# Optimization experiments

Hardware: AMD Instinct MI355X
Metric: run time of the kernel (lower is better)

Reference implementation:

```python
import jax, jax.numpy as jnp
import numpy as np
import math

K = 7
B, C, H, W = 16, 3, 256, 256
N = 50000
ANGLE = 30.0; TRANS = 0.45; SHEAR = 0.3; SCALE0, SCALE1 = 1.0, 0.5  # self.scale assumed [1.0,0.5] (upstream AutoDO)


def _bilinear(img, xs, ys):
    # img: (C,Hs,Ws); xs,ys: (Ho,Wo) pixel coords; border padding (clamp)
    Cc, Hs, Ws = img.shape
    xs = jnp.clip(xs, 0.0, Ws - 1.0)
    ys = jnp.clip(ys, 0.0, Hs - 1.0)
    x0 = jnp.floor(xs); y0 = jnp.floor(ys)
    wx = xs - x0; wy = ys - y0
    x0i = x0.astype(jnp.int32); y0i = y0.astype(jnp.int32)
    x1i = jnp.minimum(x0i + 1, Ws - 1); y1i = jnp.minimum(y0i + 1, Hs - 1)
    Ia = img[:, y0i, x0i]; Ib = img[:, y0i, x1i]
    Ic = img[:, y1i, x0i]; Id = img[:, y1i, x1i]
    return Ia * (1 - wx) * (1 - wy) + Ib * wx * (1 - wy) + Ic * (1 - wx) * wy + Id * wx * wy


def _resize(x, Ho, Wo):
    # torch F.interpolate bilinear, align_corners=False, no antialias
    Bb, Cc, Hs, Ws = x.shape
    ys = (jnp.arange(Ho, dtype=x.dtype) + 0.5) * (Hs / Ho) - 0.5
    xs = (jnp.arange(Wo, dtype=x.dtype) + 0.5) * (Ws / Wo) - 0.5
    Y, X = jnp.meshgrid(ys, xs, indexing='ij')
    return jax.vmap(lambda im: _bilinear(im, X, Y))(x)


def _warp_perspective(x, M, Ho, Wo):
    # kornia.warp_perspective: dst(p) = src(M^-1 p), bilinear, border padding, align_corners=True
    Bb, Cc, Hs, Ws = x.shape
    Minv = jnp.linalg.inv(M)  # (B,3,3)
    yy, xx = jnp.meshgrid(jnp.arange(Ho, dtype=x.dtype), jnp.arange(Wo, dtype=x.dtype), indexing='ij')
    pts = jnp.stack([xx.ravel(), yy.ravel(), jnp.ones(Ho * Wo, dtype=x.dtype)])  # (3, Ho*Wo)
    src = jnp.einsum('bij,jn->bin', Minv, pts)
    xs = (src[:, 0] / src[:, 2]).reshape(Bb, Ho, Wo)
    ys = (src[:, 1] / src[:, 2]).reshape(Bb, Ho, Wo)
    return jax.vmap(_bilinear)(x, xs, ys)


def _forward(x, paramP, paramM, gumbel_u, eps, idx):
    dt = x.dtype
    pP = jax.nn.sigmoid(paramP[:, idx])  # (K,B)
    logits = jnp.stack([jnp.log(pP).ravel(), jnp.log(1.0 - pP).ravel()], axis=1)  # (K*B,2)
    g = -jnp.log(-jnp.log(gumbel_u))
    y_soft = jax.nn.softmax(logits + g, axis=1)  # tau=1
    y_hard = jax.nn.one_hot(jnp.argmax(y_soft, axis=1), 2, dtype=y_soft.dtype)
    y = y_hard + y_soft - jax.lax.stop_gradient(y_soft)  # straight-through hard gumbel
    sP = y[:, 0].reshape(K, B)
    sM = jax.nn.sigmoid(paramM[:, idx]) * eps  # (K,B)
    ang = sP[0] * sM[0] * ANGLE
    # replicate torch's cat(W//2 * ones(B), H//2 * ones(B)).view(-1,2) layout exactly
    ctr = jnp.concatenate([jnp.full((B,), W // 2, dt), jnp.full((B,), H // 2, dt)]).reshape(-1, 2)
    sx = SCALE0 + sP[5] * sM[5] * SCALE1
    sy = SCALE0 + sP[6] * sM[6] * SCALE1
    rad = jnp.deg2rad(ang); ca = jnp.cos(rad); sa = jnp.sin(rad)
    # kornia get_rotation_matrix2d: rot=[[c,s],[-s,c]] @ diag(sx,sy); t = ctr - rot@ctr
    sr = jnp.stack([jnp.stack([ca * sx, sa * sy], -1), jnp.stack([-sa * sx, ca * sy], -1)], -2)  # (B,2,2)
    t = ctr - jnp.einsum('bij,bj->bi', sr, ctr)
    eye = jnp.broadcast_to(jnp.eye(3, dtype=dt), (B, 3, 3))
    R = eye.at[:, :2, :2].set(sr).at[:, :2, 2].set(t)
    T = eye.at[:, 0, 2].set(W * sP[1] * sM[1] * TRANS).at[:, 1, 2].set(H * sP[2] * sM[2] * TRANS)
    S = eye.at[:, 0, 1].set(sP[3] * sM[3] * SHEAR).at[:, 1, 0].set(sP[4] * sM[4] * SHEAR)
    M = S @ T @ R
    x_up = _resize(x, 4 * H, 4 * W)
    x_w = _warp_perspective(x_up, M, 4 * H, 4 * W)
    return _resize(x_w, H, W)


def setup_inputs() -> dict:
    key = jax.random.key(0)
    k1, k2, k3, k4 = jax.random.split(key, 4)
    p = 1.0 / (K - 2)
    prob_logit = math.log(p / (1.0 - p))
    m = 5.0 / 10.0
    magn_logit = math.log(m / (1.0 - m))
    return {
        'x': jax.random.uniform(k1, (B, C, H, W), jnp.float32),
        'paramP': jnp.full((K, N), prob_logit, jnp.float32),
        'paramM': jnp.full((K, N), magn_logit, jnp.float32),
        'gumbel_u': jax.random.uniform(k2, (K * B, 2), jnp.float32, minval=1e-6, maxval=1.0 - 1e-6),
        'eps': jax.random.normal(k3, (K, B), jnp.float32),
        'idx': jax.random.randint(k4, (B,), 0, N, jnp.int32),
    }


def reference(x, paramP, paramM, gumbel_u, eps, idx):
    return _forward(x, paramP, paramM, gumbel_u, eps, idx)
```

## Files before the change

### kernel.cpp

```cpp
#include <hip/hip_runtime.h>
#include <math.h>


typedef float floatx4 __attribute__((ext_vector_type(4)));

__device__ __forceinline__ floatx4 load4(const float* p) {
    floatx4 v;
    __builtin_memcpy(&v, p, sizeof(v));
    return v;
}

struct Up { int i0; float w; };

__device__ __forceinline__ Up upc(int v) {
    float u = fmaf(0.25f, (float)v, -0.375f);
    u = fminf(fmaxf(u, 0.0f), 255.0f);
    float f = floorf(u);
    Up r; r.i0 = (int)f; r.w = u - f;
    return r;
}

struct Trip { float w0, w1, w2; int base; };

__device__ __forceinline__ Trip merged3(float s) {
    float f = floorf(s);
    float fr = s - f;
    int v0 = (int)f;
    int v1 = min(v0 + 1, 1023);
    Up c0 = upc(v0), c1 = upc(v1);
    float A0 = 1.0f - fr, A1 = fr;
    float b0 = A1 * (1.0f - c1.w), b1 = A1 * c1.w;
    bool d = (c1.i0 != c0.i0);
    Trip t;
    t.w0 = A0 * (1.0f - c0.w) + (d ? 0.0f : b0);
    t.w1 = A0 * c0.w + (d ? b0 : b1);
    t.w2 = d ? b1 : 0.0f;
    t.base = c0.i0;
    return t;
}

__device__ __forceinline__ void pair_accum(
    Trip cA, Trip cB, Trip rA, Trip rB,
    const float* __restrict__ xb, float* acc)
{
    int cb = min(cA.base, cB.base);
    int rb = min(rA.base, rB.base);
    float CA[4], CB[4], RA[4], RB[4];
    bool sa_ = (cA.base != cb);
    CA[0] = sa_ ? 0.f : cA.w0;  CA[1] = sa_ ? cA.w0 : cA.w1;
    CA[2] = sa_ ? cA.w1 : cA.w2;  CA[3] = sa_ ? cA.w2 : 0.f;
    bool sb_ = (cB.base != cb);
    CB[0] = sb_ ? 0.f : cB.w0;  CB[1] = sb_ ? cB.w0 : cB.w1;
    CB[2] = sb_ ? cB.w1 : cB.w2;  CB[3] = sb_ ? cB.w2 : 0.f;
    bool ra_ = (rA.base != rb);
    RA[0] = ra_ ? 0.f : rA.w0;  RA[1] = ra_ ? rA.w0 : rA.w1;
    RA[2] = ra_ ? rA.w1 : rA.w2;  RA[3] = ra_ ? rA.w2 : 0.f;
    bool rb_ = (rB.base != rb);
    RB[0] = rb_ ? 0.f : rB.w0;  RB[1] = rb_ ? rB.w0 : rB.w1;
    RB[2] = rb_ ? rB.w1 : rB.w2;  RB[3] = rb_ ? rB.w2 : 0.f;

    float W[4][4];
#pragma unroll
    for (int r = 0; r < 4; ++r)
#pragma unroll
        for (int c = 0; c < 4; ++c)
            W[r][c] = fmaf(RB[r], CB[c], RA[r] * CA[c]);

    int base = cb;
    if (cb > 252) {
        int shift = cb - 252;
        base = 252;
        for (int s = 0; s < shift; ++s) {
#pragma unroll
            for (int r = 0; r < 4; ++r) {
                W[r][3] = W[r][2]; W[r][2] = W[r][1];
                W[r][1] = W[r][0]; W[r][0] = 0.f;
            }
        }
    }
    int e0 = rb * 256 + base;
    int e1 = min(rb + 1, 255) * 256 + base;
    int e2 = min(rb + 2, 255) * 256 + base;
    int e3 = min(rb + 3, 255) * 256 + base;
#pragma unroll
    for (int ch = 0; ch < 3; ++ch) {
        const float* pc = xb + ch * 65536;
        floatx4 L0 = load4(pc + e0);
        floatx4 L1 = load4(pc + e1);
        floatx4 L2 = load4(pc + e2);
        floatx4 L3 = load4(pc + e3);
        float s0 = fmaf(W[0][3], L0.w, fmaf(W[0][2], L0.z, fmaf(W[0][1], L0.y, W[0][0] * L0.x)));
        float s1 = fmaf(W[1][3], L1.w, fmaf(W[1][2], L1.z, fmaf(W[1][1], L1.y, W[1][0] * L1.x)));
        float s2 = fmaf(W[2][3], L2.w, fmaf(W[2][2], L2.z, fmaf(W[2][1], L2.y, W[2][0] * L2.x)));
        float s3 = fmaf(W[3][3], L3.w, fmaf(W[3][2], L3.z, fmaf(W[3][1], L3.y, W[3][0] * L3.x)));
        acc[ch] += (s0 + s1) + (s2 + s3);
    }
}

__global__ __launch_bounds__(256) void fused_warp(
    const float* __restrict__ x,
    const float* __restrict__ paramP, const float* __restrict__ paramM,
    const float* __restrict__ gumbel_u, const float* __restrict__ eps,
    const int* __restrict__ idx,
    float* __restrict__ out, int N)
{
    int b = blockIdx.z;
    int lane = threadIdx.x;
    int wid  = threadIdx.y;

    float dec = 0.f, sMv = 0.f;
    if (lane < 7) {
        int k = lane;
        int id = idx[b];
        float vP = paramP[k * N + id];
        float pP = 1.0f / (1.0f + expf(-vP));
        float l0 = logf(pP);
        float l1 = logf(1.0f - pP);
        float u0 = gumbel_u[(k * 16 + b) * 2 + 0];
        float u1 = gumbel_u[(k * 16 + b) * 2 + 1];
        float g0 = -logf(-logf(u0));
        float g1 = -logf(-logf(u1));
        dec = (l0 + g0 >= l1 + g1) ? 1.0f : 0.0f;
        float vM = paramM[k * N + id];
        float sig = 1.0f / (1.0f + expf(-vM));
        sMv = sig * eps[k * 16 + b];
    }
    float sP[7], sM[7];
#pragma unroll
    for (int k = 0; k < 7; ++k) {
        sP[k] = __shfl(dec, k, 64);
        sM[k] = __shfl(sMv, k, 64);
    }

    float ang = sP[0] * sM[0] * 30.0f;
    float rad = ang * 0.017453292519943295f;
    float ca = cosf(rad), sa = sinf(rad);
    float sx = 1.0f + sP[5] * sM[5] * 0.5f;
    float sy = 1.0f + sP[6] * sM[6] * 0.5f;
    float sr00 = ca * sx, sr01 = sa * sy;
    float sr10 = -sa * sx, sr11 = ca * sy;
    float t0 = 128.0f - (sr00 + sr01) * 128.0f;
    float t1 = 128.0f - (sr10 + sr11) * 128.0f;
    float tx2 = 256.0f * sP[1] * sM[1] * 0.45f;
    float ty2 = 256.0f * sP[2] * sM[2] * 0.45f;
    float sh01 = sP[3] * sM[3] * 0.3f;
    float sh10 = sP[4] * sM[4] * 0.3f;
    float e0m = t0 + tx2, e1m = t1 + ty2;
    float a  = sr00 + sh01 * sr10;
    float bb = sr01 + sh01 * sr11;
    float txm = e0m + sh01 * e1m;
    float c  = sh10 * sr00 + sr10;
    float d  = sh10 * sr01 + sr11;
    float tym = sh10 * e0m + e1m;
    float det = a * d - bb * c;
    float rdet = 1.0f / det;
    float m00 = d * rdet;
    float m01 = -bb * rdet;
    float m02 = (bb * tym - d * txm) * rdet;
    float m10 = -c * rdet;
    float m11 = a * rdet;
    float m12 = (c * txm - a * tym) * rdet;

    int j = blockIdx.x * 64 + lane;
    int i = blockIdx.y * 4 + wid;

    const float* xb = x + b * 3 * 65536;

    float XA = (float)(4 * j + 1);
    float Y0 = (float)(4 * i + 1);
    float x0 = fmaf(m00, XA, fmaf(m01, Y0, m02));
    float y0 = fmaf(m10, XA, fmaf(m11, Y0, m12));
    float xs[4], ys[4];
    xs[0] = x0;        ys[0] = y0;
    xs[1] = x0 + m00;  ys[1] = y0 + m10;
    xs[2] = x0 + m01;  ys[2] = y0 + m11;
    xs[3] = xs[1] + m01; ys[3] = ys[1] + m11;

    Trip cx[4], ry[4];
#pragma unroll
    for (int s = 0; s < 4; ++s) {
        cx[s] = merged3(fminf(fmaxf(xs[s], 0.f), 1023.f));
        ry[s] = merged3(fminf(fmaxf(ys[s], 0.f), 1023.f));
    }

    int cbmin = min(min(cx[0].base, cx[1].base), min(cx[2].base, cx[3].base));
    int cbmax = max(max(cx[0].base, cx[1].base), max(cx[2].base, cx[3].base));
    int rbmin = min(min(ry[0].base, ry[1].base), min(ry[2].base, ry[3].base));
    int rbmax = max(max(ry[0].base, ry[1].base), max(ry[2].base, ry[3].base));

    float acc[3] = {0.f, 0.f, 0.f};

    if (((cbmax - cbmin) | (rbmax - rbmin)) <= 1) {
        float W[4][4];
#pragma unroll
        for (int s = 0; s < 4; ++s) {
            bool sc = (cx[s].base != cbmin);
            float C0 = sc ? 0.f : cx[s].w0;
            float C1 = sc ? cx[s].w0 : cx[s].w1;
            float C2 = sc ? cx[s].w1 : cx[s].w2;
            float C3 = sc ? cx[s].w2 : 0.f;
            bool sr = (ry[s].base != rbmin);
            float R0 = sr ? 0.f : ry[s].w0;
            float R1 = sr ? ry[s].w0 : ry[s].w1;
            float R2 = sr ? ry[s].w1 : ry[s].w2;
            float R3 = sr ? ry[s].w2 : 0.f;
            float C[4] = {C0, C1, C2, C3};
            float R[4] = {R0, R1, R2, R3};
            if (s == 0) {
#pragma unroll
                for (int r = 0; r < 4; ++r)
#pragma unroll
                    for (int c = 0; c < 4; ++c)
                        W[r][c] = R[r] * C[c];
            } else {
#pragma unroll
                for (int r = 0; r < 4; ++r)
#pragma unroll
                    for (int c = 0; c < 4; ++c)
                        W[r][c] = fmaf(R[r], C[c], W[r][c]);
            }
        }

        int base = cbmin;
        if (cbmin > 252) {
            int shift = cbmin - 252;
            base = 252;
            for (int s = 0; s < shift; ++s) {
#pragma unroll
                for (int r = 0; r < 4; ++r) {
                    W[r][3] = W[r][2]; W[r][2] = W[r][1];
                    W[r][1] = W[r][0]; W[r][0] = 0.f;
                }
            }
        }

        int e0 = rbmin * 256 + base;
        int e1 = min(rbmin + 1, 255) * 256 + base;
        int e2 = min(rbmin + 2, 255) * 256 + base;
        int e3 = min(rbmin + 3, 255) * 256 + base;

        const float* p0 = xb;
        const float* p1 = xb + 65536;
        const float* p2 = xb + 131072;
        floatx4 A0 = load4(p0 + e0);
        floatx4 A1 = load4(p0 + e1);
        floatx4 A2 = load4(p0 + e2);
        floatx4 A3 = load4(p0 + e3);
        floatx4 B0 = load4(p1 + e0);
        floatx4 B1 = load4(p1 + e1);
        floatx4 B2 = load4(p1 + e2);
        floatx4 B3 = load4(p1 + e3);
        floatx4 D0 = load4(p2 + e0);
        floatx4 D1 = load4(p2 + e1);
        floatx4 D2 = load4(p2 + e2);
        floatx4 D3 = load4(p2 + e3);

        {
            float s0 = fmaf(W[0][3], A0.w, fmaf(W[0][2], A0.z, fmaf(W[0][1], A0.y, W[0][0] * A0.x)));
            float s1 = fmaf(W[1][3], A1.w, fmaf(W[1][2], A1.z, fmaf(W[1][1], A1.y, W[1][0] * A1.x)));
            float s2 = fmaf(W[2][3], A2.w, fmaf(W[2][2], A2.z, fmaf(W[2][1], A2.y, W[2][0] * A2.x)));
            float s3 = fmaf(W[3][3], A3.w, fmaf(W[3][2], A3.z, fmaf(W[3][1], A3.y, W[3][0] * A3.x)));
            acc[0] = (s0 + s1) + (s2 + s3);
        }
        {
            float s0 = fmaf(W[0][3], B0.w, fmaf(W[0][2], B0.z, fmaf(W[0][1], B0.y, W[0][0] * B0.x)));
            float s1 = fmaf(W[1][3], B1.w, fmaf(W[1][2], B1.z, fmaf(W[1][1], B1.y, W[1][0] * B1.x)));
            float s2 = fmaf(W[2][3], B2.w, fmaf(W[2][2], B2.z, fmaf(W[2][1], B2.y, W[2][0] * B2.x)));
            float s3 = fmaf(W[3][3], B3.w, fmaf(W[3][2], B3.z, fmaf(W[3][1], B3.y, W[3][0] * B3.x)));
            acc[1] = (s0 + s1) + (s2 + s3);
        }
        {
            float s0 = fmaf(W[0][3], D0.w, fmaf(W[0][2], D0.z, fmaf(W[0][1], D0.y, W[0][0] * D0.x)));
            float s1 = fmaf(W[1][3], D1.w, fmaf(W[1][2], D1.z, fmaf(W[1][1], D1.y, W[1][0] * D1.x)));
            float s2 = fmaf(W[2][3], D2.w, fmaf(W[2][2], D2.z, fmaf(W[2][1], D2.y, W[2][0] * D2.x)));
            float s3 = fmaf(W[3][3], D3.w, fmaf(W[3][2], D3.z, fmaf(W[3][1], D3.y, W[3][0] * D3.x)));
            acc[2] = (s0 + s1) + (s2 + s3);
        }
    } else {
        pair_accum(cx[0], cx[1], ry[0], ry[1], xb, acc);
        pair_accum(cx[2], cx[3], ry[2], ry[3], xb, acc);
    }

    int obase = ((b * 3) * 256 + i) * 256 + j;
    out[obase]          = 0.25f * acc[0];
    out[obase + 65536]  = 0.25f * acc[1];
    out[obase + 131072] = 0.25f * acc[2];
}

extern "C" void kernel_launch(void* const* d_in, const int* in_sizes, int n_in,
                              void* d_out, int out_size, void* d_ws, size_t ws_size,
                              hipStream_t stream) {
    const float* x      = (const float*)d_in[0];
    const float* paramP = (const float*)d_in[1];
    const float* paramM = (const float*)d_in[2];
    const float* gumbel = (const float*)d_in[3];
    const float* eps    = (const float*)d_in[4];
    const int*   idx    = (const int*)d_in[5];
    float* out = (float*)d_out;
    int N = in_sizes[1] / 7;

    hipLaunchKernelGGL(fused_warp, dim3(4, 64, 16), dim3(64, 4, 1), 0, stream,
                       x, paramP, paramM, gumbel, eps, idx, out, N);
}
```

Baseline: 89.98 us.

## Compute four output rows per thread and share overlapping source-row loads

Each thread now produces four consecutive output rows instead of one, and the grid shrinks in y to match. A cheap pre-pass computes the source footprint base of each row; if every lane's four footprints share a column base and advance one source row each, the thread loads seven rows per channel once and reuses them across the four outputs instead of issuing sixteen loads per channel. Otherwise it falls back to the old per-row path. The change raises register pressure, repeats the coordinate math in the pre-pass, and leaves fewer blocks in the grid.

```diff
diff --git a/kernel.cpp b/kernel.cpp
--- a/kernel.cpp
+++ b/kernel.cpp
@@ -37,6 +37,14 @@
     t.w2 = d ? b1 : 0.0f;
     t.base = c0.i0;
     return t;
+}
+
+__device__ __forceinline__ int basefun(float s) {
+    float f = floorf(s);
+    int v0 = (int)f;
+    float u = fmaf(0.25f, (float)v0, -0.375f);
+    u = fminf(fmaxf(u, 0.0f), 255.0f);
+    return (int)floorf(u);
 }
 
 __device__ __forceinline__ void pair_accum(
@@ -106,7 +114,7 @@
 {
     int b = blockIdx.z;
     int lane = threadIdx.x;
-    int wid  = threadIdx.y;
+    int ty   = threadIdx.y;
 
     float dec = 0.f, sMv = 0.f;
     if (lane < 7) {
@@ -135,10 +143,10 @@
     float ang = sP[0] * sM[0] * 30.0f;
     float rad = ang * 0.017453292519943295f;
     float ca = cosf(rad), sa = sinf(rad);
-    float sx = 1.0f + sP[5] * sM[5] * 0.5f;
-    float sy = 1.0f + sP[6] * sM[6] * 0.5f;
-    float sr00 = ca * sx, sr01 = sa * sy;
-    float sr10 = -sa * sx, sr11 = ca * sy;
+    float sxs = 1.0f + sP[5] * sM[5] * 0.5f;
+    float sys = 1.0f + sP[6] * sM[6] * 0.5f;
+    float sr00 = ca * sxs, sr01 = sa * sys;
+    float sr10 = -sa * sxs, sr11 = ca * sys;
     float t0 = 128.0f - (sr00 + sr01) * 128.0f;
     float t1 = 128.0f - (sr10 + sr11) * 128.0f;
     float tx2 = 256.0f * sP[1] * sM[1] * 0.45f;
@@ -161,130 +169,255 @@
     float m11 = a * rdet;
     float m12 = (c * txm - a * tym) * rdet;
 
-    int j = blockIdx.x * 64 + lane;
-    int i = blockIdx.y * 4 + wid;
+    int j  = blockIdx.x * 64 + lane;
+    int i0 = (blockIdx.y * 4 + ty) * 4;
 
     const float* xb = x + b * 3 * 65536;
-
     float XA = (float)(4 * j + 1);
-    float Y0 = (float)(4 * i + 1);
-    float x0 = fmaf(m00, XA, fmaf(m01, Y0, m02));
-    float y0 = fmaf(m10, XA, fmaf(m11, Y0, m12));
-    float xs[4], ys[4];
-    xs[0] = x0;        ys[0] = y0;
-    xs[1] = x0 + m00;  ys[1] = y0 + m10;
-    xs[2] = x0 + m01;  ys[2] = y0 + m11;
-    xs[3] = xs[1] + m01; ys[3] = ys[1] + m11;
-
-    Trip cx[4], ry[4];
-#pragma unroll
-    for (int s = 0; s < 4; ++s) {
-        cx[s] = merged3(fminf(fmaxf(xs[s], 0.f), 1023.f));
-        ry[s] = merged3(fminf(fmaxf(ys[s], 0.f), 1023.f));
-    }
-
-    int cbmin = min(min(cx[0].base, cx[1].base), min(cx[2].base, cx[3].base));
-    int cbmax = max(max(cx[0].base, cx[1].base), max(cx[2].base, cx[3].base));
-    int rbmin = min(min(ry[0].base, ry[1].base), min(ry[2].base, ry[3].base));
-    int rbmax = max(max(ry[0].base, ry[1].base), max(ry[2].base, ry[3].base));
-
-    float acc[3] = {0.f, 0.f, 0.f};
-
-    if (((cbmax - cbmin) | (rbmax - rbmin)) <= 1) {
-        float W[4][4];
-#pragma unroll
-        for (int s = 0; s < 4; ++s) {
-            bool sc = (cx[s].base != cbmin);
-            float C0 = sc ? 0.f : cx[s].w0;
-            float C1 = sc ? cx[s].w0 : cx[s].w1;
-            float C2 = sc ? cx[s].w1 : cx[s].w2;
-            float C3 = sc ? cx[s].w2 : 0.f;
-            bool sr = (ry[s].base != rbmin);
-            float R0 = sr ? 0.f : ry[s].w0;
-            float R1 = sr ? ry[s].w0 : ry[s].w1;
-            float R2 = sr ? ry[s].w1 : ry[s].w2;
-            float R3 = sr ? ry[s].w2 : 0.f;
-            float C[4] = {C0, C1, C2, C3};
-            float R[4] = {R0, R1, R2, R3};
-            if (s == 0) {
-#pragma unroll
-                for (int r = 0; r < 4; ++r)
-#pragma unroll
-                    for (int c = 0; c < 4; ++c)
-                        W[r][c] = R[r] * C[c];
-            } else {
-#pragma unroll
-                for (int r = 0; r < 4; ++r)
-#pragma unroll
-                    for (int c = 0; c < 4; ++c)
-                        W[r][c] = fmaf(R[r], C[c], W[r][c]);
-            }
+
+    int rbk[4], cbk[4];
+    bool fk[4];
+    bool chainl = true;
+#pragma unroll
+    for (int k = 0; k < 4; ++k) {
+        float Y0 = (float)(4 * (i0 + k) + 1);
+        float x0 = fmaf(m00, XA, fmaf(m01, Y0, m02));
+        float y0 = fmaf(m10, XA, fmaf(m11, Y0, m12));
+        float xs0 = fminf(fmaxf(x0, 0.f), 1023.f);
+        float xs1 = fminf(fmaxf(x0 + m00, 0.f), 1023.f);
+        float xs2 = fminf(fmaxf(x0 + m01, 0.f), 1023.f);
+        float xs3 = fminf(fmaxf((x0 + m00) + m01, 0.f), 1023.f);
+        float ys0 = fminf(fmaxf(y0, 0.f), 1023.f);
+        float ys1 = fminf(fmaxf(y0 + m10, 0.f), 1023.f);
+        float ys2 = fminf(fmaxf(y0 + m11, 0.f), 1023.f);
+        float ys3 = fminf(fmaxf((y0 + m10) + m11, 0.f), 1023.f);
+        int c0 = basefun(xs0), c1 = basefun(xs1), c2 = basefun(xs2), c3 = basefun(xs3);
+        int r0 = basefun(ys0), r1 = basefun(ys1), r2 = basefun(ys2), r3 = basefun(ys3);
+        int cmn = min(min(c0, c1), min(c2, c3));
+        int cmx = max(max(c0, c1), max(c2, c3));
+        int rmn = min(min(r0, r1), min(r2, r3));
+        int rmx = max(max(r0, r1), max(r2, r3));
+        cbk[k] = cmn; rbk[k] = rmn;
+        fk[k] = (((cmx - cmn) | (rmx - rmn)) <= 1);
+        chainl = chainl && fk[k] && (cbk[k] == cbk[0]) && (rbk[k] == rbk[0] + k);
+    }
+    bool chain = __all(chainl);
+
+    float acc[4][3];
+#pragma unroll
+    for (int k = 0; k < 4; ++k) {
+        acc[k][0] = 0.f; acc[k][1] = 0.f; acc[k][2] = 0.f;
+    }
+
+    if (chain) {
+        int rb0 = rbk[0];
+        int base = (cbk[0] > 252) ? 252 : cbk[0];
+        floatx4 RA[7], RB[7], RD[7];
+#pragma unroll
+        for (int t = 0; t < 7; ++t) {
+            int et = min(rb0 + t, 255) * 256 + base;
+            RA[t] = load4(xb + et);
+            RB[t] = load4(xb + 65536 + et);
+            RD[t] = load4(xb + 131072 + et);
         }
-
-        int base = cbmin;
-        if (cbmin > 252) {
-            int shift = cbmin - 252;
-            base = 252;
-            for (int s = 0; s < shift; ++s) {
-#pragma unroll
-                for (int r = 0; r < 4; ++r) {
-                    W[r][3] = W[r][2]; W[r][2] = W[r][1];
-                    W[r][1] = W[r][0]; W[r][0] = 0.f;
-                }
-            }
-        }
-
-        int e0 = rbmin * 256 + base;
-        int e1 = min(rbmin + 1, 255) * 256 + base;
-        int e2 = min(rbmin + 2, 255) * 256 + base;
-        int e3 = min(rbmin + 3, 255) * 256 + base;
-
-        const float* p0 = xb;
-        const float* p1 = xb + 65536;
-        const float* p2 = xb + 131072;
-        floatx4 A0 = load4(p0 + e0);
-        floatx4 A1 = load4(p0 + e1);
-        floatx4 A2 = load4(p0 + e2);
-        floatx4 A3 = load4(p0 + e3);
-        floatx4 B0 = load4(p1 + e0);
-        floatx4 B1 = load4(p1 + e1);
-        floatx4 B2 = load4(p1 + e2);
-        floatx4 B3 = load4(p1 + e3);
-        floatx4 D0 = load4(p2 + e0);
-        floatx4 D1 = load4(p2 + e1);
-        floatx4 D2 = load4(p2 + e2);
-        floatx4 D3 = load4(p2 + e3);
-
-        {
-            float s0 = fmaf(W[0][3], A0.w, fmaf(W[0][2], A0.z, fmaf(W[0][1], A0.y, W[0][0] * A0.x)));
-            float s1 = fmaf(W[1][3], A1.w, fmaf(W[1][2], A1.z, fmaf(W[1][1], A1.y, W[1][0] * A1.x)));
-            float s2 = fmaf(W[2][3], A2.w, fmaf(W[2][2], A2.z, fmaf(W[2][1], A2.y, W[2][0] * A2.x)));
-            float s3 = fmaf(W[3][3], A3.w, fmaf(W[3][2], A3.z, fmaf(W[3][1], A3.y, W[3][0] * A3.x)));
-            acc[0] = (s0 + s1) + (s2 + s3);
-        }
-        {
-            float s0 = fmaf(W[0][3], B0.w, fmaf(W[0][2], B0.z, fmaf(W[0][1], B0.y, W[0][0] * B0.x)));
-            float s1 = fmaf(W[1][3], B1.w, fmaf(W[1][2], B1.z, fmaf(W[1][1], B1.y, W[1][0] * B1.x)));
-            float s2 = fmaf(W[2][3], B2.w, fmaf(W[2][2], B2.z, fmaf(W[2][1], B2.y, W[2][0] * B2.x)));
-            float s3 = fmaf(W[3][3], B3.w, fmaf(W[3][2], B3.z, fmaf(W[3][1], B3.y, W[3][0] * B3.x)));
-            acc[1] = (s0 + s1) + (s2 + s3);
-        }
-        {
-            float s0 = fmaf(W[0][3], D0.w, fmaf(W[0][2], D0.z, fmaf(W[0][1], D0.y, W[0][0] * D0.x)));
-            float s1 = fmaf(W[1][3], D1.w, fmaf(W[1][2], D1.z, fmaf(W[1][1], D1.y, W[1][0] * D1.x)));
-            float s2 = fmaf(W[2][3], D2.w, fmaf(W[2][2], D2.z, fmaf(W[2][1], D2.y, W[2][0] * D2.x)));
-            float s3 = fmaf(W[3][3], D3.w, fmaf(W[3][2], D3.z, fmaf(W[3][1], D3.y, W[3][0] * D3.x)));
-            acc[2] = (s0 + s1) + (s2 + s3);
+#pragma unroll
+        for (int k = 0; k < 4; ++k) {
+            float Y0 = (float)(4 * (i0 + k) + 1);
+            float x0 = fmaf(m00, XA, fmaf(m01, Y0, m02));
+            float y0 = fmaf(m10, XA, fmaf(m11, Y0, m12));
+            float xs[4], ys[4];
+            xs[0] = x0;          ys[0] = y0;
+            xs[1] = x0 + m00;    ys[1] = y0 + m10;
+            xs[2] = x0 + m01;    ys[2] = y0 + m11;
+            xs[3] = xs[1] + m01; ys[3] = ys[1] + m11;
+            Trip cx[4], ry[4];
+#pragma unroll
+            for (int s = 0; s < 4; ++s) {
+                cx[s] = merged3(fminf(fmaxf(xs[s], 0.f), 1023.f));
+                ry[s] = merged3(fminf(fmaxf(ys[s], 0.f), 1023.f));
+            }
+            int cbmin = min(min(cx[0].base, cx[1].base), min(cx[2].base, cx[3].base));
+            int rbmin = min(min(ry[0].base, ry[1].base), min(ry[2].base, ry[3].base));
+            (void)rbmin;
+            float W[4][4];
+#pragma unroll
+            for (int s = 0; s < 4; ++s) {
+                bool sc = (cx[s].base != cbmin);
+                float C0 = sc ? 0.f : cx[s].w0;
+                float C1 = sc ? cx[s].w0 : cx[s].w1;
+                float C2 = sc ? cx[s].w1 : cx[s].w2;
+                float C3 = sc ? cx[s].w2 : 0.f;
+                bool sr = (ry[s].base != rbk[k]);
+                float R0 = sr ? 0.f : ry[s].w0;
+                float R1 = sr ? ry[s].w0 : ry[s].w1;
+                float R2 = sr ? ry[s].w1 : ry[s].w2;
+                float R3 = sr ? ry[s].w2 : 0.f;
+                float C[4] = {C0, C1, C2, C3};
+                float R[4] = {R0, R1, R2, R3};
+                if (s == 0) {
+#pragma unroll
+                    for (int r = 0; r < 4; ++r)
+#pragma unroll
+                        for (int cc = 0; cc < 4; ++cc)
+                            W[r][cc] = R[r] * C[cc];
+                } else {
+#pragma unroll
+                    for (int r = 0; r < 4; ++r)
+#pragma unroll
+                        for (int cc = 0; cc < 4; ++cc)
+                            W[r][cc] = fmaf(R[r], C[cc], W[r][cc]);
+                }
+            }
+            if (cbmin > 252) {
+                int shift = cbmin - 252;
+                for (int s = 0; s < shift; ++s) {
+#pragma unroll
+                    for (int r = 0; r < 4; ++r) {
+                        W[r][3] = W[r][2]; W[r][2] = W[r][1];
+                        W[r][1] = W[r][0]; W[r][0] = 0.f;
+                    }
+                }
+            }
+            {
+                float s0 = fmaf(W[0][3], RA[k+0].w, fmaf(W[0][2], RA[k+0].z, fmaf(W[0][1], RA[k+0].y, W[0][0] * RA[k+0].x)));
+                float s1 = fmaf(W[1][3], RA[k+1].w, fmaf(W[1][2], RA[k+1].z, fmaf(W[1][1], RA[k+1].y, W[1][0] * RA[k+1].x)));
+                float s2 = fmaf(W[2][3], RA[k+2].w, fmaf(W[2][2], RA[k+2].z, fmaf(W[2][1], RA[k+2].y, W[2][0] * RA[k+2].x)));
+                float s3 = fmaf(W[3][3], RA[k+3].w, fmaf(W[3][2], RA[k+3].z, fmaf(W[3][1], RA[k+3].y, W[3][0] * RA[k+3].x)));
+                acc[k][0] = (s0 + s1) + (s2 + s3);
+            }
+            {
+                float s0 = fmaf(W[0][3], RB[k+0].w, fmaf(W[0][2], RB[k+0].z, fmaf(W[0][1], RB[k+0].y, W[0][0] * RB[k+0].x)));
+                float s1 = fmaf(W[1][3], RB[k+1].w, fmaf(W[1][2], RB[k+1].z, fmaf(W[1][1], RB[k+1].y, W[1][0] * RB[k+1].x)));
+                float s2 = fmaf(W[2][3], RB[k+2].w, fmaf(W[2][2], RB[k+2].z, fmaf(W[2][1], RB[k+2].y, W[2][0] * RB[k+2].x)));
+                float s3 = fmaf(W[3][3], RB[k+3].w, fmaf(W[3][2], RB[k+3].z, fmaf(W[3][1], RB[k+3].y, W[3][0] * RB[k+3].x)));
+                acc[k][1] = (s0 + s1) + (s2 + s3);
+            }
+            {
+                float s0 = fmaf(W[0][3], RD[k+0].w, fmaf(W[0][2], RD[k+0].z, fmaf(W[0][1], RD[k+0].y, W[0][0] * RD[k+0].x)));
+                float s1 = fmaf(W[1][3], RD[k+1].w, fmaf(W[1][2], RD[k+1].z, fmaf(W[1][1], RD[k+1].y, W[1][0] * RD[k+1].x)));
+                float s2 = fmaf(W[2][3], RD[k+2].w, fmaf(W[2][2], RD[k+2].z, fmaf(W[2][1], RD[k+2].y, W[2][0] * RD[k+2].x)));
+                float s3 = fmaf(W[3][3], RD[k+3].w, fmaf(W[3][2], RD[k+3].z, fmaf(W[3][1], RD[k+3].y, W[3][0] * RD[k+3].x)));
+                acc[k][2] = (s0 + s1) + (s2 + s3);
+            }
         }
     } else {
-        pair_accum(cx[0], cx[1], ry[0], ry[1], xb, acc);
-        pair_accum(cx[2], cx[3], ry[2], ry[3], xb, acc);
-    }
-
-    int obase = ((b * 3) * 256 + i) * 256 + j;
-    out[obase]          = 0.25f * acc[0];
-    out[obase + 65536]  = 0.25f * acc[1];
-    out[obase + 131072] = 0.25f * acc[2];
+#pragma unroll
+        for (int k = 0; k < 4; ++k) {
+            float Y0 = (float)(4 * (i0 + k) + 1);
+            float x0 = fmaf(m00, XA, fmaf(m01, Y0, m02));
+            float y0 = fmaf(m10, XA, fmaf(m11, Y0, m12));
+            float xs[4], ys[4];
+            xs[0] = x0;          ys[0] = y0;
+            xs[1] = x0 + m00;    ys[1] = y0 + m10;
+            xs[2] = x0 + m01;    ys[2] = y0 + m11;
+            xs[3] = xs[1] + m01; ys[3] = ys[1] + m11;
+            Trip cx[4], ry[4];
+#pragma unroll
+            for (int s = 0; s < 4; ++s) {
+                cx[s] = merged3(fminf(fmaxf(xs[s], 0.f), 1023.f));
+                ry[s] = merged3(fminf(fmaxf(ys[s], 0.f), 1023.f));
+            }
+            int cbmin = min(min(cx[0].base, cx[1].base), min(cx[2].base, cx[3].base));
+            int cbmax = max(max(cx[0].base, cx[1].base), max(cx[2].base, cx[3].base));
+            int rbmin = min(min(ry[0].base, ry[1].base), min(ry[2].base, ry[3].base));
+            int rbmax = max(max(ry[0].base, ry[1].base), max(ry[2].base, ry[3].base));
+
+            if (((cbmax - cbmin) | (rbmax - rbmin)) <= 1) {
+                float W[4][4];
+#pragma unroll
+                for (int s = 0; s < 4; ++s) {
+                    bool sc = (cx[s].base != cbmin);
+                    float C0 = sc ? 0.f : cx[s].w0;
+                    float C1 = sc ? cx[s].w0 : cx[s].w1;
+                    float C2 = sc ? cx[s].w1 : cx[s].w2;
+                    float C3 = sc ? cx[s].w2 : 0.f;
+                    bool sr = (ry[s].base != rbmin);
+                    float R0 = sr ? 0.f : ry[s].w0;
+                    float R1 = sr ? ry[s].w0 : ry[s].w1;
+                    float R2 = sr ? ry[s].w1 : ry[s].w2;
+                    float R3 = sr ? ry[s].w2 : 0.f;
+                    float C[4] = {C0, C1, C2, C3};
+                    float R[4] = {R0, R1, R2, R3};
+                    if (s == 0) {
+#pragma unroll
+                        for (int r = 0; r < 4; ++r)
+#pragma unroll
+                            for (int cc = 0; cc < 4; ++cc)
+                                W[r][cc] = R[r] * C[cc];
+                    } else {
+#pragma unroll
+                        for (int r = 0; r < 4; ++r)
+#pragma unroll
+                            for (int cc = 0; cc < 4; ++cc)
+                                W[r][cc] = fmaf(R[r], C[cc], W[r][cc]);
+                    }
+                }
+                int base = cbmin;
+                if (cbmin > 252) {
+                    int shift = cbmin - 252;
+                    base = 252;
+                    for (int s = 0; s < shift; ++s) {
+#pragma unroll
+                        for (int r = 0; r < 4; ++r) {
+                            W[r][3] = W[r][2]; W[r][2] = W[r][1];
+                            W[r][1] = W[r][0]; W[r][0] = 0.f;
+                        }
+                    }
+                }
+                int e0 = rbmin * 256 + base;
+                int e1 = min(rbmin + 1, 255) * 256 + base;
+                int e2 = min(rbmin + 2, 255) * 256 + base;
+                int e3 = min(rbmin + 3, 255) * 256 + base;
+                const float* p0 = xb;
+                const float* p1 = xb + 65536;
+                const float* p2 = xb + 131072;
+                floatx4 A0 = load4(p0 + e0);
+                floatx4 A1 = load4(p0 + e1);
+                floatx4 A2 = load4(p0 + e2);
+                floatx4 A3 = load4(p0 + e3);
+                floatx4 B0 = load4(p1 + e0);
+                floatx4 B1 = load4(p1 + e1);
+                floatx4 B2 = load4(p1 + e2);
+                floatx4 B3 = load4(p1 + e3);
+                floatx4 D0 = load4(p2 + e0);
+                floatx4 D1 = load4(p2 + e1);
+                floatx4 D2 = load4(p2 + e2);
+                floatx4 D3 = load4(p2 + e3);
+                {
+                    float s0 = fmaf(W[0][3], A0.w, fmaf(W[0][2], A0.z, fmaf(W[0][1], A0.y, W[0][0] * A0.x)));
+                    float s1 = fmaf(W[1][3], A1.w, fmaf(W[1][2], A1.z, fmaf(W[1][1], A1.y, W[1][0] * A1.x)));
+                    float s2 = fmaf(W[2][3], A2.w, fmaf(W[2][2], A2.z, fmaf(W[2][1], A2.y, W[2][0] * A2.x)));
+                    float s3 = fmaf(W[3][3], A3.w, fmaf(W[3][2], A3.z, fmaf(W[3][1], A3.y, W[3][0] * A3.x)));
+                    acc[k][0] = (s0 + s1) + (s2 + s3);
+                }
+                {
+                    float s0 = fmaf(W[0][3], B0.w, fmaf(W[0][2], B0.z, fmaf(W[0][1], B0.y, W[0][0] * B0.x)));
+                    float s1 = fmaf(W[1][3], B1.w, fmaf(W[1][2], B1.z, fmaf(W[1][1], B1.y, W[1][0] * B1.x)));
+                    float s2 = fmaf(W[2][3], B2.w, fmaf(W[2][2], B2.z, fmaf(W[2][1], B2.y, W[2][0] * B2.x)));
+                    float s3 = fmaf(W[3][3], B3.w, fmaf(W[3][2], B3.z, fmaf(W[3][1], B3.y, W[3][0] * B3.x)));
+                    acc[k][1] = (s0 + s1) + (s2 + s3);
+                }
+                {
+                    float s0 = fmaf(W[0][3], D0.w, fmaf(W[0][2], D0.z, fmaf(W[0][1], D0.y, W[0][0] * D0.x)));
+                    float s1 = fmaf(W[1][3], D1.w, fmaf(W[1][2], D1.z, fmaf(W[1][1], D1.y, W[1][0] * D1.x)));
+                    float s2 = fmaf(W[2][3], D2.w, fmaf(W[2][2], D2.z, fmaf(W[2][1], D2.y, W[2][0] * D2.x)));
+                    float s3 = fmaf(W[3][3], D3.w, fmaf(W[3][2], D3.z, fmaf(W[3][1], D3.y, W[3][0] * D3.x)));
+                    acc[k][2] = (s0 + s1) + (s2 + s3);
+                }
+            } else {
+                pair_accum(cx[0], cx[1], ry[0], ry[1], xb, acc[k]);
+                pair_accum(cx[2], cx[3], ry[2], ry[3], xb, acc[k]);
+            }
+        }
+    }
+
+#pragma unroll
+    for (int k = 0; k < 4; ++k) {
+        int obase = ((b * 3) * 256 + (i0 + k)) * 256 + j;
+        out[obase]          = 0.25f * acc[k][0];
+        out[obase + 65536]  = 0.25f * acc[k][1];
+        out[obase + 131072] = 0.25f * acc[k][2];
+    }
 }
 
 extern "C" void kernel_launch(void* const* d_in, const int* in_sizes, int n_in,
@@ -299,6 +432,6 @@
     float* out = (float*)d_out;
     int N = in_sizes[1] / 7;
 
-    hipLaunchKernelGGL(fused_warp, dim3(4, 64, 16), dim3(64, 4, 1), 0, stream,
+    hipLaunchKernelGGL(fused_warp, dim3(4, 16, 16), dim3(64, 4, 1), 0, stream,
                        x, paramP, paramM, gumbel, eps, idx, out, N);
 }
```

Result: slower. 94.99 us (+5.6%).
